# Optimization experiments

Measured on AMD Instinct MI355X. Metric: run time of the kernel, lower is better.

## Reference

```python
import jax, jax.numpy as jnp
import numpy as np

B, L, D, TK = 64, 48, 256, 128
T = 2 * L - 1  # L shifts + (L-1) reduces


def setup_inputs() -> dict:
    key = jax.random.key(0)
    ks = jax.random.split(key, 9)
    s = 0.05
    inp = {
        "buf_h": jax.random.normal(ks[0], (B, L, D), jnp.float32),
        "buf_c": jax.random.normal(ks[1], (B, L, D), jnp.float32),
        # Tracker weights: buf/stack1/stack2 (size -> 4*tracker_size, no bias), lateral (tk -> 4*tk, bias)
        "Wb": jax.random.normal(ks[2], (D, 4 * TK), jnp.float32) * s,
        "W1": jax.random.normal(ks[3], (D, 4 * TK), jnp.float32) * s,
        "W2": jax.random.normal(ks[4], (D, 4 * TK), jnp.float32) * s,
        "Wl": jax.random.normal(ks[5], (TK, 4 * TK), jnp.float32) * s,
        "bl": jnp.zeros((4 * TK,), jnp.float32),
        # Reduce (TreeLSTM) weights: left (size->5*size, bias), right (no bias), track (tk->5*size, no bias)
        "WL": jax.random.normal(ks[6], (D, 5 * D), jnp.float32) * s,
        "bL": jnp.zeros((5 * D,), jnp.float32),
        "WR": jax.random.normal(ks[7], (D, 5 * D), jnp.float32) * s,
        "WT": jax.random.normal(ks[8], (TK, 5 * D), jnp.float32) * s,
    }
    # Valid full-length transition sequence per example: S S (R S)*(L-2) R  -> SHIFT=0, REDUCE=1
    pat = np.array([0, 0] + [1, 0] * (L - 2) + [1], dtype=np.int32)
    inp["transitions"] = jnp.asarray(np.tile(pat[None], (B, 1)))  # [B, T]
    return inp


def _lstm(c, gates):
    # tracker LSTM cell: gates chunk into (a, i, f, o)
    a, i, f, o = jnp.split(gates, 4, axis=-1)
    c2 = jnp.tanh(a) * jax.nn.sigmoid(i) + jax.nn.sigmoid(f) * c
    h2 = jax.nn.sigmoid(o) * jnp.tanh(c2)
    return c2, h2


def _treelstm(c1, c2, gates):
    # Reduce composition: gates chunk into (a, i, f1, f2, o)
    a, i, f1, f2, o = jnp.split(gates, 5, axis=-1)
    c = jnp.tanh(a) * jax.nn.sigmoid(i) + jax.nn.sigmoid(f1) * c1 + jax.nn.sigmoid(f2) * c2
    h = jax.nn.sigmoid(o) * jnp.tanh(c)
    return h, c


def _spinn_forward(buf_h, buf_c, transitions, Wb, W1, W2, Wl, bl, WL, bL, WR, WT):
    Bn, Ln, Dn = buf_h.shape
    Tn = transitions.shape[1]
    bidx = jnp.arange(Bn)
    stack0 = jnp.zeros((Bn, Ln, 2 * Dn), buf_h.dtype)  # each slot holds [h; c]
    sp0 = jnp.zeros((Bn,), jnp.int32)  # stack depth
    bp0 = jnp.zeros((Bn,), jnp.int32)  # buffer read pointer
    th0 = jnp.zeros((Bn, Wl.shape[0]), buf_h.dtype)
    tc0 = jnp.zeros_like(th0)

    def top(stack_, sp_, k):
        # k-th item from the top, zeros if depth < k (matches explicit zero-padding)
        idx = jnp.clip(sp_ - k, 0, Ln - 1)
        v = stack_[bidx, idx]
        return jnp.where((sp_ >= k)[:, None], v, jnp.zeros_like(v))

    def step(carry, xs):
        stack, sp, bp, th, tc = carry
        t, trans = xs
        shift = (trans == 0)
        bp_safe = jnp.clip(bp, 0, Ln - 1)
        buf_ok = (bp < Ln)[:, None]
        tb_h = jnp.where(buf_ok, buf_h[bidx, bp_safe], 0.0)  # top-of-buffer h
        s1 = top(stack, sp, 1)
        s2 = top(stack, sp, 2)
        s1h, s1c = s1[:, :Dn], s1[:, Dn:]
        s2h, s2c = s2[:, :Dn], s2[:, Dn:]
        # Tracker: sum of three bias-free linears (+ lateral with bias after step 0)
        gates = tb_h @ Wb + s1h @ W1 + s2h @ W2
        gates = gates + jnp.where(t > 0, th @ Wl + bl, 0.0)
        tc2, th2 = _lstm(tc, gates)
        # Reduce: right = top of stack, left = second item; tracking = new tracker h
        rgates = s2h @ WL + bL + s1h @ WR + th2 @ WT
        rh, rc = _treelstm(s2c, s1c, rgates)
        reduced = jnp.concatenate([rh, rc], axis=-1)
        # Shift: push [h;c] from buffer
        tb_c = jnp.where(buf_ok, buf_c[bidx, bp_safe], 0.0)
        shifted = jnp.concatenate([tb_h, tb_c], axis=-1)
        newval = jnp.where(shift[:, None], shifted, reduced)
        pos = jnp.where(shift, sp, jnp.maximum(sp - 2, 0))
        stack = stack.at[bidx, pos].set(newval)
        sp = jnp.where(shift, sp + 1, jnp.maximum(sp - 1, 0))
        bp = bp + shift.astype(bp.dtype)
        return (stack, sp, bp, th2, tc2), None

    (stack, sp, bp, th, tc), _ = jax.lax.scan(
        step, (stack0, sp0, bp0, th0, tc0),
        (jnp.arange(Tn), transitions.T))
    final = stack[bidx, jnp.clip(sp - 1, 0, Ln - 1)]  # [B, 2D] = [h; c] of root
    return final


def reference(buf_h, buf_c, transitions, Wb, W1, W2, Wl, bl, WL, bL, WR, WT):
    return _spinn_forward(buf_h, buf_c, transitions, Wb, W1, W2, Wl, bl, WL, bL, WR, WT)
```

## Files before the change

### kernel.cpp

```cpp
#include <hip/hip_runtime.h>
#include <cstdint>
#include <cstddef>

#define NB 64
#define LN 48
#define DN 256
#define TKN 128
#define TN 95
#define RMAX 48
#define GA 512
#define GR 1280
#define NWG 256
#define NT 512

__device__ __forceinline__ float sigf(float x) { return 1.0f / (1.0f + expf(-x)); }

__device__ __forceinline__ float bf2f(unsigned u16) {
    unsigned x = u16 << 16;
    return __builtin_bit_cast(float, x);
}
__device__ __forceinline__ unsigned short f2bf(float f) {
    unsigned x = __builtin_bit_cast(unsigned, f);
    unsigned r = (x + 0x7FFFu + ((x >> 16) & 1u)) >> 16;
    return (unsigned short)r;
}

__device__ __forceinline__ float cohLd(const float* p) {
    return __hip_atomic_load(p, __ATOMIC_RELAXED, __HIP_MEMORY_SCOPE_AGENT);
}
__device__ __forceinline__ void cohSt(float* p, float v) {
    __hip_atomic_store(p, v, __ATOMIC_RELAXED, __HIP_MEMORY_SCOPE_AGENT);
}
__device__ __forceinline__ unsigned cohLdU(const unsigned* p) {
    return __hip_atomic_load(p, __ATOMIC_RELAXED, __HIP_MEMORY_SCOPE_AGENT);
}
__device__ __forceinline__ void cohStU(unsigned* p, unsigned v) {
    __hip_atomic_store(p, v, __ATOMIC_RELAXED, __HIP_MEMORY_SCOPE_AGENT);
}

__device__ __forceinline__ void qsync(unsigned* slots, int grp, unsigned& qph) {
    __syncthreads();
    qph += 1;
    if (threadIdx.x == 0) cohStU(&slots[blockIdx.x * 16], qph);
    if (threadIdx.x < 16) {
        while (cohLdU(&slots[(grp * 16 + threadIdx.x) * 16]) < qph)
            __builtin_amdgcn_s_sleep(1);
    }
    asm volatile("" ::: "memory");
    __syncthreads();
}

__device__ __forceinline__ void psync(unsigned* slotsP, int u, int xcd, unsigned& pph) {
    __syncthreads();
    pph += 1;
    if (threadIdx.x == 0) cohStU(&slotsP[(u * 8 + xcd) * 16], pph);
    if (threadIdx.x < 8) {
        while (cohLdU(&slotsP[(u * 8 + threadIdx.x) * 16]) < pph)
            __builtin_amdgcn_s_sleep(1);
    }
    asm volatile("" ::: "memory");
    __syncthreads();
}

__global__ void k_sched(const int* __restrict__ trans,
                        int* __restrict__ tbcode, int* __restrict__ s1code,
                        int* __restrict__ s2code, int* __restrict__ wkA,
                        int* __restrict__ fcode, int* __restrict__ anyred) {
    __shared__ int tg[NB][LN];
    int b = threadIdx.x;
    if (b >= NB) return;
    for (int i = 0; i < LN; ++i) tg[b][i] = -1;
    int sp = 0, bp = 0, k = 0;
    for (int t = 0; t < TN; ++t) {
        int tr = trans[b * TN + t];
        int shift = (tr == 0);
        int tb = (bp < LN) ? bp : -1;
        tbcode[t * NB + b] = tb;
        int i1 = sp - 1; if (i1 < 0) i1 = 0; if (i1 > LN - 1) i1 = LN - 1;
        int i2 = sp - 2; if (i2 < 0) i2 = 0; if (i2 > LN - 1) i2 = LN - 1;
        s1code[t * NB + b] = (sp >= 1) ? tg[b][i1] : -1;
        s2code[t * NB + b] = (sp >= 2) ? tg[b][i2] : -1;
        int wk_t;
        if (shift) {
            wk_t = -1;
            if (sp >= 0 && sp < LN) tg[b][sp] = tb;
            sp = sp + 1;
            bp = bp + 1;
        } else {
            wk_t = k;
            int pos = sp - 2; if (pos < 0) pos = 0;
            if (pos < LN) tg[b][pos] = 1000 + k;
            k++;
            sp = sp - 1; if (sp < 0) sp = 0;
        }
        wkA[t * NB + b] = wk_t;
        unsigned long long m = __ballot(wk_t >= 0);
        if (b == 0) anyred[t] = (m != 0ull) ? 1 : 0;
    }
    int fi = sp - 1; if (fi < 0) fi = 0; if (fi > LN - 1) fi = LN - 1;
    fcode[b] = tg[b][fi];
}

__global__ __launch_bounds__(256) void k_pack_a(
    const float* __restrict__ Wb, const float* __restrict__ W1,
    const float* __restrict__ W2, const float* __restrict__ Wl,
    const float* __restrict__ blv,
    unsigned short* __restrict__ WAb, float* __restrict__ blA) {
    int idx = blockIdx.x * 256 + threadIdx.x;
    if (idx < 8 * 896 * 64) {
        int s = idx / (896 * 64);
        int r = idx % (896 * 64);
        int k = r >> 6, c = r & 63;
        int p = s * 64 + c;
        int j = p >> 2, q = p & 3;
        int sc = q * 128 + j;
        float v;
        if (k < 256)      v = Wb[(size_t)k * GA + sc];
        else if (k < 512) v = W1[(size_t)(k - 256) * GA + sc];
        else if (k < 768) v = W2[(size_t)(k - 512) * GA + sc];
        else              v = Wl[(size_t)(k - 768) * GA + sc];
        WAb[idx] = f2bf(v);
    }
    if (idx < 512) {
        int j = idx >> 2, q = idx & 3;
        blA[idx] = blv[q * 128 + j];
    }
}

__global__ __launch_bounds__(256) void k_pack_b(
    const float* __restrict__ WLm, const float* __restrict__ WRm,
    const float* __restrict__ WTm, unsigned short* __restrict__ WBb) {
    int idx = blockIdx.x * 256 + threadIdx.x;
    if (idx >= 16 * 640 * 128) return;
    int s = idx / (640 * 128);
    int r = idx % (640 * 128);
    int k = r >> 7, cc = r & 127;
    int jj = cc >> 3, g = cc & 7;
    float v = 0.f;
    if (g < 5) {
        int sc = g * 256 + s * 16 + jj;
        if (k < 256)      v = WLm[(size_t)k * GR + sc];
        else if (k < 512) v = WRm[(size_t)(k - 256) * GR + sc];
        else              v = WTm[(size_t)(k - 512) * GR + sc];
    }
    WBb[idx] = f2bf(v);
}

__global__ __launch_bounds__(NT, 1) void k_spinn(
    const float* __restrict__ bufh, const float* __restrict__ bufc,
    const unsigned short* __restrict__ WAb, const float* __restrict__ blA,
    const unsigned short* __restrict__ WBb, const float* __restrict__ bLv,
    const int* __restrict__ tbcode, const int* __restrict__ s1code,
    const int* __restrict__ s2code, const int* __restrict__ wkA,
    const int* __restrict__ fcode, const int* __restrict__ anyred,
    float* __restrict__ th, float* __restrict__ tc,
    float* __restrict__ redh, float* __restrict__ redc,
    unsigned* __restrict__ slots, unsigned* __restrict__ slotsP,
    float* __restrict__ out) {
    const int wg = blockIdx.x;
    const int tid = threadIdx.x;
    const int lane = tid & 63;
    const int w = tid >> 6;
    unsigned qph = 0, pph = 0;

    const int xcd = wg & 7;
    const int u = wg >> 3;
    const int grp = wg >> 4;
    const int jg = xcd;
    const int bg1 = u;
    const int bg2 = u >> 1;
    const int jgw = (u & 1) + 2 * xcd;

    __shared__ float xs[2][896];
    __shared__ float part1[2][64][33];
    __shared__ float gsum[2][64];
    __shared__ float xs2[4][16][33];
    __shared__ float part2[16][16][21];
    __shared__ float gsum2[4][5][16];
    __shared__ float xst[4][128];

    for (int t = 0; t < TN; ++t) {
        const int par = t & 1;
        const bool red = anyred[t] != 0;

        int ngroups = red ? 960 : 448;
        for (int g = tid; g < ngroups; g += NT) {
            if (g < 448) {
                int row = g & 1, k0 = (g >> 1) * 4;
                int b = bg1 * 2 + row;
                float4 v = {0.f, 0.f, 0.f, 0.f};
                if (k0 < 256) {
                    int c = tbcode[t * NB + b];
                    if (c >= 0) v = *(const float4*)&bufh[((size_t)b * LN + c) * DN + k0];
                } else if (k0 < 512) {
                    int c = s1code[t * NB + b];
                    int kk = k0 - 256;
                    if (c >= 1000) {
                        const float* p = &redh[((size_t)(c - 1000) * NB + b) * DN + kk];
                        v.x = cohLd(p); v.y = cohLd(p + 1); v.z = cohLd(p + 2); v.w = cohLd(p + 3);
                    } else if (c >= 0) v = *(const float4*)&bufh[((size_t)b * LN + c) * DN + kk];
                } else if (k0 < 768) {
                    int c = s2code[t * NB + b];
                    int kk = k0 - 512;
                    if (c >= 1000) {
                        const float* p = &redh[((size_t)(c - 1000) * NB + b) * DN + kk];
                        v.x = cohLd(p); v.y = cohLd(p + 1); v.z = cohLd(p + 2); v.w = cohLd(p + 3);
                    } else if (c >= 0) v = *(const float4*)&bufh[((size_t)b * LN + c) * DN + kk];
                } else {
                    const float* p = &th[((size_t)par * NB + b) * TKN + (k0 - 768)];
                    v.x = cohLd(p); v.y = cohLd(p + 1); v.z = cohLd(p + 2); v.w = cohLd(p + 3);
                }
                *(float4*)&xs[row][k0] = v;
            } else {
                int g2 = g - 448;
                int row = g2 & 3, k0 = (g2 >> 2) * 4;
                int b = bg2 * 4 + row;
                float4 v = {0.f, 0.f, 0.f, 0.f};
                if (k0 < 256) {
                    int c = s2code[t * NB + b];
                    if (c >= 1000) {
                        const float* p = &redh[((size_t)(c - 1000) * NB + b) * DN + k0];
                        v.x = cohLd(p); v.y = cohLd(p + 1); v.z = cohLd(p + 2); v.w = cohLd(p + 3);
                    } else if (c >= 0) v = *(const float4*)&bufh[((size_t)b * LN + c) * DN + k0];
                } else {
                    int c = s1code[t * NB + b];
                    int kk = k0 - 256;
                    if (c >= 1000) {
                        const float* p = &redh[((size_t)(c - 1000) * NB + b) * DN + kk];
                        v.x = cohLd(p); v.y = cohLd(p + 1); v.z = cohLd(p + 2); v.w = cohLd(p + 3);
                    } else if (c >= 0) v = *(const float4*)&bufh[((size_t)b * LN + c) * DN + kk];
                }
                *(float4*)&xs2[row][k0 >> 5][k0 & 31] = v;
            }
        }
        __syncthreads();

        float acc[5][4];
        if (w < 4) {
            int c8 = lane & 7, kq = lane >> 3;
            int kbase = w * 224;
            const uint4* wp = (const uint4*)WAb + ((size_t)(jg * 896 + kbase + kq) * 8) + c8;
            float a0[8], a1[8];
            #pragma unroll
            for (int cc = 0; cc < 8; ++cc) { a0[cc] = 0.f; a1[cc] = 0.f; }
            #pragma unroll 4
            for (int i = 0; i < 28; ++i) {
                uint4 wv = wp[(size_t)i * 64];
                int k = kbase + kq + i * 8;
                float x0 = xs[0][k], x1 = xs[1][k];
                float wf0 = bf2f(wv.x & 0xFFFF), wf1 = bf2f(wv.x >> 16);
                float wf2 = bf2f(wv.y & 0xFFFF), wf3 = bf2f(wv.y >> 16);
                float wf4 = bf2f(wv.z & 0xFFFF), wf5 = bf2f(wv.z >> 16);
                float wf6 = bf2f(wv.w & 0xFFFF), wf7 = bf2f(wv.w >> 16);
                a0[0] += x0 * wf0; a1[0] += x1 * wf0;
                a0[1] += x0 * wf1; a1[1] += x1 * wf1;
                a0[2] += x0 * wf2; a1[2] += x1 * wf2;
                a0[3] += x0 * wf3; a1[3] += x1 * wf3;
                a0[4] += x0 * wf4; a1[4] += x1 * wf4;
                a0[5] += x0 * wf5; a1[5] += x1 * wf5;
                a0[6] += x0 * wf6; a1[6] += x1 * wf6;
                a0[7] += x0 * wf7; a1[7] += x1 * wf7;
            }
            int ks = w * 8 + kq;
            #pragma unroll
            for (int cc = 0; cc < 8; ++cc) {
                part1[0][c8 * 8 + cc][ks] = a0[cc];
                part1[1][c8 * 8 + cc][ks] = a1[cc];
            }
        } else if (red) {
            int t2 = tid - 256, jj = t2 & 15, ks = t2 >> 4;
            #pragma unroll
            for (int g = 0; g < 5; ++g)
                #pragma unroll
                for (int b4 = 0; b4 < 4; ++b4) acc[g][b4] = 0.f;
            const uint4* wb = (const uint4*)WBb + ((size_t)(jgw * 640 + ks * 32) * 16) + jj;
            #pragma unroll 4
            for (int i = 0; i < 32; ++i) {
                uint4 wv = wb[(size_t)i * 16];
                float w0 = bf2f(wv.x & 0xFFFF), w1 = bf2f(wv.x >> 16);
                float w2 = bf2f(wv.y & 0xFFFF), w3 = bf2f(wv.y >> 16);
                float w4 = bf2f(wv.z & 0xFFFF);
                int kb = (ks * 32 + i) >> 5, ko = i;
                float x0 = xs2[0][kb][ko], x1 = xs2[1][kb][ko];
                float x2 = xs2[2][kb][ko], x3 = xs2[3][kb][ko];
                acc[0][0] += x0 * w0; acc[1][0] += x0 * w1; acc[2][0] += x0 * w2; acc[3][0] += x0 * w3; acc[4][0] += x0 * w4;
                acc[0][1] += x1 * w0; acc[1][1] += x1 * w1; acc[2][1] += x1 * w2; acc[3][1] += x1 * w3; acc[4][1] += x1 * w4;
                acc[0][2] += x2 * w0; acc[1][2] += x2 * w1; acc[2][2] += x2 * w2; acc[3][2] += x2 * w3; acc[4][2] += x2 * w4;
                acc[0][3] += x3 * w0; acc[1][3] += x3 * w1; acc[2][3] += x3 * w2; acc[3][3] += x3 * w3; acc[4][3] += x3 * w4;
            }
        }
        __syncthreads();

        if (tid < 128) {
            int b = tid & 1, col = tid >> 1;
            float s = 0.f;
            #pragma unroll
            for (int ks = 0; ks < 32; ++ks) s += part1[b][col][ks];
            if (t > 0) s += blA[jg * 64 + col];
            gsum[b][col] = s;
        }
        __syncthreads();
        if (tid < 32) {
            int bl_ = tid >> 4, jj = tid & 15;
            int b = bg1 * 2 + bl_;
            int j = jg * 16 + jj;
            float4 g4 = *(const float4*)&gsum[bl_][jj * 4];
            float tco = tc[((size_t)par * NB + b) * TKN + j];
            float c2v = tanhf(g4.x) * sigf(g4.y) + sigf(g4.z) * tco;
            float h2 = sigf(g4.w) * tanhf(c2v);
            tc[((size_t)(par ^ 1) * NB + b) * TKN + j] = c2v;
            cohSt(&th[((size_t)(par ^ 1) * NB + b) * TKN + j], h2);
        }

        if (!red) {
            psync(slotsP, u, xcd, pph);
            continue;
        }
        qsync(slots, grp, qph);

        {
            int b4 = tid >> 7, kk = tid & 127;
            xst[b4][kk] = cohLd(&th[((size_t)(par ^ 1) * NB + bg2 * 4 + b4) * TKN + kk]);
        }
        __syncthreads();
        if (w >= 4) {
            int t2 = tid - 256, jj = t2 & 15, ks = t2 >> 4;
            const uint4* wb = (const uint4*)WBb + ((size_t)(jgw * 640 + 512 + ks * 8) * 16) + jj;
            #pragma unroll
            for (int i = 0; i < 8; ++i) {
                uint4 wv = wb[(size_t)i * 16];
                float w0 = bf2f(wv.x & 0xFFFF), w1 = bf2f(wv.x >> 16);
                float w2 = bf2f(wv.y & 0xFFFF), w3 = bf2f(wv.y >> 16);
                float w4 = bf2f(wv.z & 0xFFFF);
                int kk2 = ks * 8 + i;
                float x0 = xst[0][kk2], x1 = xst[1][kk2], x2 = xst[2][kk2], x3 = xst[3][kk2];
                acc[0][0] += x0 * w0; acc[1][0] += x0 * w1; acc[2][0] += x0 * w2; acc[3][0] += x0 * w3; acc[4][0] += x0 * w4;
                acc[0][1] += x1 * w0; acc[1][1] += x1 * w1; acc[2][1] += x1 * w2; acc[3][1] += x1 * w3; acc[4][1] += x1 * w4;
                acc[0][2] += x2 * w0; acc[1][2] += x2 * w1; acc[2][2] += x2 * w2; acc[3][2] += x2 * w3; acc[4][2] += x2 * w4;
                acc[0][3] += x3 * w0; acc[1][3] += x3 * w1; acc[2][3] += x3 * w2; acc[3][3] += x3 * w3; acc[4][3] += x3 * w4;
            }
            #pragma unroll
            for (int g = 0; g < 5; ++g)
                #pragma unroll
                for (int b4 = 0; b4 < 4; ++b4)
                    part2[ks][jj][g * 4 + b4] = acc[g][b4];
        }
        __syncthreads();
        if (tid < 320) {
            int g = tid >> 6, r = tid & 63;
            int bl_ = r >> 4, jj = r & 15;
            float s = 0.f;
            #pragma unroll
            for (int ks = 0; ks < 16; ++ks) s += part2[ks][jj][g * 4 + bl_];
            gsum2[bl_][g][jj] = s;
        }
        __syncthreads();
        if (tid < 64) {
            int bl_ = tid >> 4, jj = tid & 15;
            int b = bg2 * 4 + bl_;
            int wk = wkA[t * NB + b];
            if (wk >= 0) {
                int j = jgw * 16 + jj;
                float ga  = gsum2[bl_][0][jj] + bLv[0 * 256 + j];
                float gi  = gsum2[bl_][1][jj] + bLv[1 * 256 + j];
                float gf1 = gsum2[bl_][2][jj] + bLv[2 * 256 + j];
                float gf2 = gsum2[bl_][3][jj] + bLv[3 * 256 + j];
                float go  = gsum2[bl_][4][jj] + bLv[4 * 256 + j];
                int c1 = s1code[t * NB + b], c2 = s2code[t * NB + b];
                float s2cv = (c2 == -1) ? 0.f
                            : ((c2 >= 1000) ? redc[((size_t)(c2 - 1000) * NB + b) * DN + j]
                                            : bufc[((size_t)b * LN + c2) * DN + j]);
                float s1cv = (c1 == -1) ? 0.f
                            : ((c1 >= 1000) ? redc[((size_t)(c1 - 1000) * NB + b) * DN + j]
                                            : bufc[((size_t)b * LN + c1) * DN + j]);
                float cc = tanhf(ga) * sigf(gi) + sigf(gf1) * s2cv + sigf(gf2) * s1cv;
                float hh = sigf(go) * tanhf(cc);
                cohSt(&redh[((size_t)wk * NB + b) * DN + j], hh);
                redc[((size_t)wk * NB + b) * DN + j] = cc;
            }
        }
        qsync(slots, grp, qph);
    }

    if (tid < 64) {
        int bl_ = tid >> 4, jj = tid & 15;
        int b = bg2 * 4 + bl_;
        int j = jgw * 16 + jj;
        int c = fcode[b];
        float h = 0.f, cv = 0.f;
        if (c >= 1000) {
            h  = cohLd(&redh[((size_t)(c - 1000) * NB + b) * DN + j]);
            cv = redc[((size_t)(c - 1000) * NB + b) * DN + j];
        } else if (c >= 0) {
            h  = bufh[((size_t)b * LN + c) * DN + j];
            cv = bufc[((size_t)b * LN + c) * DN + j];
        }
        out[(size_t)b * 2 * DN + j]      = h;
        out[(size_t)b * 2 * DN + DN + j] = cv;
    }
}

extern "C" void kernel_launch(void* const* d_in, const int* in_sizes, int n_in,
                              void* d_out, int out_size, void* d_ws, size_t ws_size,
                              hipStream_t stream) {
    const float* bufh = (const float*)d_in[0];
    const float* bufc = (const float*)d_in[1];
    const float* Wb   = (const float*)d_in[2];
    const float* W1   = (const float*)d_in[3];
    const float* W2   = (const float*)d_in[4];
    const float* Wl   = (const float*)d_in[5];
    const float* blv  = (const float*)d_in[6];
    const float* WLm  = (const float*)d_in[7];
    const float* bLv  = (const float*)d_in[8];
    const float* WR   = (const float*)d_in[9];
    const float* WT   = (const float*)d_in[10];
    const int* trans  = (const int*)d_in[11];
    float* out = (float*)d_out;

    char* p = (char*)d_ws;
    auto carve = [&](size_t bytes) -> char* {
        char* r = p;
        p += (bytes + 255) & ~(size_t)255;
        return r;
    };
    int* tbcode = (int*)carve((size_t)TN * NB * 4);
    int* s1code = (int*)carve((size_t)TN * NB * 4);
    int* s2code = (int*)carve((size_t)TN * NB * 4);
    int* wkA    = (int*)carve((size_t)TN * NB * 4);
    int* fcode  = (int*)carve((size_t)NB * 4);
    int* anyred = (int*)carve((size_t)TN * 4);
    float* th   = (float*)carve((size_t)2 * NB * TKN * 4);
    float* tc   = (float*)carve((size_t)2 * NB * TKN * 4);
    float* redh = (float*)carve((size_t)RMAX * NB * DN * 4);
    float* redc = (float*)carve((size_t)RMAX * NB * DN * 4);
    unsigned short* WAb = (unsigned short*)carve((size_t)8 * 896 * 64 * 2);
    float* blA  = (float*)carve((size_t)512 * 4);
    unsigned short* WBb = (unsigned short*)carve((size_t)16 * 640 * 128 * 2);
    unsigned* slots  = (unsigned*)carve((size_t)NWG * 16 * 4);
    unsigned* slotsP = (unsigned*)carve((size_t)NWG * 16 * 4);

    hipMemsetAsync(th, 0, (size_t)2 * NB * TKN * 4, stream);
    hipMemsetAsync(tc, 0, (size_t)2 * NB * TKN * 4, stream);
    hipMemsetAsync(slots, 0, (size_t)NWG * 16 * 4, stream);
    hipMemsetAsync(slotsP, 0, (size_t)NWG * 16 * 4, stream);

    k_sched<<<1, 64, 0, stream>>>(trans, tbcode, s1code, s2code, wkA, fcode, anyred);
    k_pack_a<<<(8 * 896 * 64 + 255) / 256, 256, 0, stream>>>(Wb, W1, W2, Wl, blv, WAb, blA);
    k_pack_b<<<(16 * 640 * 128 + 255) / 256, 256, 0, stream>>>(WLm, WR, WT, WBb);
    k_spinn<<<NWG, NT, 0, stream>>>(bufh, bufc, WAb, blA, WBb, bLv,
                                    tbcode, s1code, s2code, wkA, fcode, anyred,
                                    th, tc, redh, redc, slots, slotsP, out);
}
```

Baseline: 827.9 us.

## Split tracker GEMV across all waves on shift steps and prefetch reduce cells

On steps with no reduce, the four idle waves now share the tracker GEMV by splitting the K loop in half, with partial sums written into a widened part1 buffer. On reduce steps, the stack cell values needed by the TreeLSTM are gathered into shared memory during the initial load phase, so the post-sync epilogue no longer makes dependent global loads. The reduce partial sums are also written to part2 before the second barrier and the tracking-term contribution is accumulated into them afterwards, so the th load and the write overlap. The cost is extra shared memory, more load groups per step, and read-modify-write traffic on part2.

Measured after the change: 721.0 us (median of 2 runs). 12.9% less time.

```diff
diff --git a/kernel.cpp b/kernel.cpp
--- a/kernel.cpp
+++ b/kernel.cpp
@@ -172,18 +172,19 @@
     const int jgw = (u & 1) + 2 * xcd;
 
     __shared__ float xs[2][896];
-    __shared__ float part1[2][64][33];
+    __shared__ float part1[2][64][65];
     __shared__ float gsum[2][64];
     __shared__ float xs2[4][16][33];
     __shared__ float part2[16][16][21];
     __shared__ float gsum2[4][5][16];
     __shared__ float xst[4][128];
+    __shared__ float cellv[2][4][17];
 
     for (int t = 0; t < TN; ++t) {
         const int par = t & 1;
         const bool red = anyred[t] != 0;
 
-        int ngroups = red ? 960 : 448;
+        int ngroups = red ? 1088 : 448;
         for (int g = tid; g < ngroups; g += NT) {
             if (g < 448) {
                 int row = g & 1, k0 = (g >> 1) * 4;
@@ -211,7 +212,7 @@
                     v.x = cohLd(p); v.y = cohLd(p + 1); v.z = cohLd(p + 2); v.w = cohLd(p + 3);
                 }
                 *(float4*)&xs[row][k0] = v;
-            } else {
+            } else if (g < 960) {
                 int g2 = g - 448;
                 int row = g2 & 3, k0 = (g2 >> 2) * 4;
                 int b = bg2 * 4 + row;
@@ -231,20 +232,35 @@
                     } else if (c >= 0) v = *(const float4*)&bufh[((size_t)b * LN + c) * DN + kk];
                 }
                 *(float4*)&xs2[row][k0 >> 5][k0 & 31] = v;
+            } else {
+                int g3 = g - 960;
+                int sel = g3 >> 6, r = g3 & 63;
+                int bl_ = r >> 4, jj = r & 15;
+                int b = bg2 * 4 + bl_;
+                int j = jgw * 16 + jj;
+                int c = (sel ? s1code : s2code)[t * NB + b];
+                float v = 0.f;
+                if (c >= 1000)   v = redc[((size_t)(c - 1000) * NB + b) * DN + j];
+                else if (c >= 0) v = bufc[((size_t)b * LN + c) * DN + j];
+                cellv[sel][bl_][jj] = v;
             }
         }
         __syncthreads();
 
         float acc[5][4];
-        if (w < 4) {
+        if (w < 4 || !red) {
+            int weff = w & 3, ihalf = w >> 2;
             int c8 = lane & 7, kq = lane >> 3;
-            int kbase = w * 224;
+            int kbase = weff * 224;
+            int i0 = red ? 0 : ihalf * 14;
+            int ni = red ? 28 : 14;
             const uint4* wp = (const uint4*)WAb + ((size_t)(jg * 896 + kbase + kq) * 8) + c8;
             float a0[8], a1[8];
             #pragma unroll
             for (int cc = 0; cc < 8; ++cc) { a0[cc] = 0.f; a1[cc] = 0.f; }
             #pragma unroll 4
-            for (int i = 0; i < 28; ++i) {
+            for (int ii = 0; ii < ni; ++ii) {
+                int i = i0 + ii;
                 uint4 wv = wp[(size_t)i * 64];
                 int k = kbase + kq + i * 8;
                 float x0 = xs[0][k], x1 = xs[1][k];
@@ -261,13 +277,13 @@
                 a0[6] += x0 * wf6; a1[6] += x1 * wf6;
                 a0[7] += x0 * wf7; a1[7] += x1 * wf7;
             }
-            int ks = w * 8 + kq;
+            int slot = weff * 8 + kq + (red ? 0 : ihalf * 32);
             #pragma unroll
             for (int cc = 0; cc < 8; ++cc) {
-                part1[0][c8 * 8 + cc][ks] = a0[cc];
-                part1[1][c8 * 8 + cc][ks] = a1[cc];
-            }
-        } else if (red) {
+                part1[0][c8 * 8 + cc][slot] = a0[cc];
+                part1[1][c8 * 8 + cc][slot] = a1[cc];
+            }
+        } else {
             int t2 = tid - 256, jj = t2 & 15, ks = t2 >> 4;
             #pragma unroll
             for (int g = 0; g < 5; ++g)
@@ -280,9 +296,8 @@
                 float w0 = bf2f(wv.x & 0xFFFF), w1 = bf2f(wv.x >> 16);
                 float w2 = bf2f(wv.y & 0xFFFF), w3 = bf2f(wv.y >> 16);
                 float w4 = bf2f(wv.z & 0xFFFF);
-                int kb = (ks * 32 + i) >> 5, ko = i;
-                float x0 = xs2[0][kb][ko], x1 = xs2[1][kb][ko];
-                float x2 = xs2[2][kb][ko], x3 = xs2[3][kb][ko];
+                float x0 = xs2[0][ks][i], x1 = xs2[1][ks][i];
+                float x2 = xs2[2][ks][i], x3 = xs2[3][ks][i];
                 acc[0][0] += x0 * w0; acc[1][0] += x0 * w1; acc[2][0] += x0 * w2; acc[3][0] += x0 * w3; acc[4][0] += x0 * w4;
                 acc[0][1] += x1 * w0; acc[1][1] += x1 * w1; acc[2][1] += x1 * w2; acc[3][1] += x1 * w3; acc[4][1] += x1 * w4;
                 acc[0][2] += x2 * w0; acc[1][2] += x2 * w1; acc[2][2] += x2 * w2; acc[3][2] += x2 * w3; acc[4][2] += x2 * w4;
@@ -296,6 +311,10 @@
             float s = 0.f;
             #pragma unroll
             for (int ks = 0; ks < 32; ++ks) s += part1[b][col][ks];
+            if (!red) {
+                #pragma unroll
+                for (int ks = 32; ks < 64; ++ks) s += part1[b][col][ks];
+            }
             if (t > 0) s += blA[jg * 64 + col];
             gsum[b][col] = s;
         }
@@ -318,13 +337,31 @@
         }
         qsync(slots, grp, qph);
 
+        float xreg;
         {
             int b4 = tid >> 7, kk = tid & 127;
-            xst[b4][kk] = cohLd(&th[((size_t)(par ^ 1) * NB + bg2 * 4 + b4) * TKN + kk]);
-        }
-        __syncthreads();
+            xreg = cohLd(&th[((size_t)(par ^ 1) * NB + bg2 * 4 + b4) * TKN + kk]);
+        }
         if (w >= 4) {
             int t2 = tid - 256, jj = t2 & 15, ks = t2 >> 4;
+            #pragma unroll
+            for (int g = 0; g < 5; ++g)
+                #pragma unroll
+                for (int b4 = 0; b4 < 4; ++b4)
+                    part2[ks][jj][g * 4 + b4] = acc[g][b4];
+        }
+        {
+            int b4 = tid >> 7, kk = tid & 127;
+            xst[b4][kk] = xreg;
+        }
+        __syncthreads();
+        if (w >= 4) {
+            int t2 = tid - 256, jj = t2 & 15, ks = t2 >> 4;
+            float wt[5][4];
+            #pragma unroll
+            for (int g = 0; g < 5; ++g)
+                #pragma unroll
+                for (int b4 = 0; b4 < 4; ++b4) wt[g][b4] = 0.f;
             const uint4* wb = (const uint4*)WBb + ((size_t)(jgw * 640 + 512 + ks * 8) * 16) + jj;
             #pragma unroll
             for (int i = 0; i < 8; ++i) {
@@ -334,16 +371,16 @@
                 float w4 = bf2f(wv.z & 0xFFFF);
                 int kk2 = ks * 8 + i;
                 float x0 = xst[0][kk2], x1 = xst[1][kk2], x2 = xst[2][kk2], x3 = xst[3][kk2];
-                acc[0][0] += x0 * w0; acc[1][0] += x0 * w1; acc[2][0] += x0 * w2; acc[3][0] += x0 * w3; acc[4][0] += x0 * w4;
-                acc[0][1] += x1 * w0; acc[1][1] += x1 * w1; acc[2][1] += x1 * w2; acc[3][1] += x1 * w3; acc[4][1] += x1 * w4;
-                acc[0][2] += x2 * w0; acc[1][2] += x2 * w1; acc[2][2] += x2 * w2; acc[3][2] += x2 * w3; acc[4][2] += x2 * w4;
-                acc[0][3] += x3 * w0; acc[1][3] += x3 * w1; acc[2][3] += x3 * w2; acc[3][3] += x3 * w3; acc[4][3] += x3 * w4;
+                wt[0][0] += x0 * w0; wt[1][0] += x0 * w1; wt[2][0] += x0 * w2; wt[3][0] += x0 * w3; wt[4][0] += x0 * w4;
+                wt[0][1] += x1 * w0; wt[1][1] += x1 * w1; wt[2][1] += x1 * w2; wt[3][1] += x1 * w3; wt[4][1] += x1 * w4;
+                wt[0][2] += x2 * w0; wt[1][2] += x2 * w1; wt[2][2] += x2 * w2; wt[3][2] += x2 * w3; wt[4][2] += x2 * w4;
+                wt[0][3] += x3 * w0; wt[1][3] += x3 * w1; wt[2][3] += x3 * w2; wt[3][3] += x3 * w3; wt[4][3] += x3 * w4;
             }
             #pragma unroll
             for (int g = 0; g < 5; ++g)
                 #pragma unroll
                 for (int b4 = 0; b4 < 4; ++b4)
-                    part2[ks][jj][g * 4 + b4] = acc[g][b4];
+                    part2[ks][jj][g * 4 + b4] += wt[g][b4];
         }
         __syncthreads();
         if (tid < 320) {
@@ -366,13 +403,8 @@
                 float gf1 = gsum2[bl_][2][jj] + bLv[2 * 256 + j];
                 float gf2 = gsum2[bl_][3][jj] + bLv[3 * 256 + j];
                 float go  = gsum2[bl_][4][jj] + bLv[4 * 256 + j];
-                int c1 = s1code[t * NB + b], c2 = s2code[t * NB + b];
-                float s2cv = (c2 == -1) ? 0.f
-                            : ((c2 >= 1000) ? redc[((size_t)(c2 - 1000) * NB + b) * DN + j]
-                                            : bufc[((size_t)b * LN + c2) * DN + j]);
-                float s1cv = (c1 == -1) ? 0.f
-                            : ((c1 >= 1000) ? redc[((size_t)(c1 - 1000) * NB + b) * DN + j]
-                                            : bufc[((size_t)b * LN + c1) * DN + j]);
+                float s2cv = cellv[0][bl_][jj];
+                float s1cv = cellv[1][bl_][jj];
                 float cc = tanhf(ga) * sigf(gi) + sigf(gf1) * s2cv + sigf(gf2) * s1cv;
                 float hh = sigf(go) * tanhf(cc);
                 cohSt(&redh[((size_t)wk * NB + b) * DN + j], hh);
```
